# Optimization experiments

Measured on AMD Instinct MI355X. Metric: run time of the kernel, lower is better.

## Reference

```python
import jax, jax.numpy as jnp
import numpy as np

B, S, H = 2, 4096, 1024
WINDOW = 32


def setup_inputs() -> dict:
    key = jax.random.key(0)
    ks = jax.random.split(key, 10)
    s = 1.0 / np.sqrt(H)
    return {
        "hidden_states": jax.random.normal(ks[0], (B, S, H), dtype=jnp.float32),
        "Wq": jax.random.normal(ks[1], (H, H), dtype=jnp.float32) * s,
        "Wk": jax.random.normal(ks[2], (H, H), dtype=jnp.float32) * s,
        "Wv": jax.random.normal(ks[3], (H, H), dtype=jnp.float32) * s,
        "Wo": jax.random.normal(ks[4], (H, H), dtype=jnp.float32) * s,
        "ln_w": jnp.ones((H,), dtype=jnp.float32),
        "ln_b": jnp.zeros((H,), dtype=jnp.float32),
        "W1": jax.random.normal(ks[5], (H // 2, H), dtype=jnp.float32) * s,
        "b1": jnp.zeros((H // 2,), dtype=jnp.float32),
        "W2": jax.random.normal(ks[6], (H, H // 2), dtype=jnp.float32) * (1.0 / np.sqrt(H // 2)),
        "b2": jnp.zeros((H,), dtype=jnp.float32),
    }


def _layernorm(x, w, b, eps=1e-5):
    mu = jnp.mean(x, axis=-1, keepdims=True)
    var = jnp.var(x, axis=-1, keepdims=True)
    return (x - mu) * jax.lax.rsqrt(var + eps) * w + b


def reference(hidden_states, Wq, Wk, Wv, Wo, ln_w, ln_b, W1, b1, W2, b2):
    x = hidden_states  # [B,S,H]
    q = x @ Wq.T
    k = x @ Wk.T
    v = x @ Wv.T
    # banded causal mask: keep j<=i and j >= i-WINDOW+1
    i = jnp.arange(S)[:, None]
    j = jnp.arange(S)[None, :]
    local_mask = (j <= i) & (j >= i - WINDOW + 1)  # [S,S] bool
    scores = jnp.einsum('bqh,bkh->bqk', q, k) / np.sqrt(H)
    scores = jnp.where(local_mask[None], scores, -jnp.inf)
    probs = jax.nn.softmax(scores, axis=-1)
    attn_out = jnp.einsum('bqk,bkh->bqh', probs, v) @ Wo.T
    draft = x + attn_out
    h = _layernorm(draft, ln_w, ln_b)
    h = jax.nn.gelu(h @ W1.T + b1, approximate=False)
    adapter_out = h @ W2.T + b2
    return draft + adapter_out
```

## Files before the change

kernel.cpp:

```cpp
#include <hip/hip_runtime.h>
#include <stdint.h>

typedef unsigned short u16;
typedef __bf16 bfx8 __attribute__((ext_vector_type(8)));
typedef float f32x4 __attribute__((ext_vector_type(4)));

__device__ __forceinline__ u16 f2bf(float x) {
    unsigned int u = __float_as_uint(x);
    u += 0x7fffu + ((u >> 16) & 1u);
    return (u16)(u >> 16);
}

__device__ __forceinline__ void async16(const void* g, void* l) {
    __builtin_amdgcn_global_load_lds(
        (const __attribute__((address_space(1))) unsigned int*)(uintptr_t)g,
        (__attribute__((address_space(3))) unsigned int*)(unsigned int)(uintptr_t)l,
        16, 0, 0);
}

__global__ __launch_bounds__(256) void cast_bf16(const float* __restrict__ in,
                                                 u16* __restrict__ out, int n8) {
    int i = blockIdx.x * 256 + threadIdx.x;
    if (i >= n8) return;
    const float4* p = (const float4*)(in + (size_t)i * 8);
    float4 a = p[0], b = p[1];
    ushort4 o0, o1;
    o0.x = f2bf(a.x); o0.y = f2bf(a.y); o0.z = f2bf(a.z); o0.w = f2bf(a.w);
    o1.x = f2bf(b.x); o1.y = f2bf(b.y); o1.z = f2bf(b.z); o1.w = f2bf(b.w);
    ushort4* q = (ushort4*)(out + (size_t)i * 8);
    q[0] = o0; q[1] = o1;
}

template <int EPI>
__global__ __launch_bounds__(256, 2)
void gemm_nt(const u16* __restrict__ A, const u16* __restrict__ Bw,
             u16* __restrict__ outb, float* __restrict__ outf,
             const float* __restrict__ res, const float* __restrict__ bias,
             int M, int N, int K) {
    __shared__ __align__(1024) unsigned char lds[32768];
    unsigned char* ldsA = lds;
    unsigned char* ldsB = lds + 16384;
    const int t = threadIdx.x;
    const int lane = t & 63, w = t >> 6;
    const int laneR = lane & 15, laneK = lane >> 4;
    const int wr = w >> 1, wc = w & 1;
    const int row0 = blockIdx.y * 128, col0 = blockIdx.x * 128;

    f32x4 acc[4][4] = {};

    int sr[4], sko[4];
#pragma unroll
    for (int c = 0; c < 4; ++c) {
        int li = c * 256 + t;
        sr[c] = li >> 3;
        sko[c] = (li & 7) ^ (sr[c] & 7);
    }

    for (int kt = 0; kt < K; kt += 64) {
#pragma unroll
        for (int c = 0; c < 4; ++c) {
            int li = c * 256 + t;
            async16(A + (size_t)(row0 + sr[c]) * K + kt + sko[c] * 8, ldsA + li * 16);
            async16(Bw + (size_t)(col0 + sr[c]) * K + kt + sko[c] * 8, ldsB + li * 16);
        }
        __syncthreads();
#pragma unroll
        for (int ks = 0; ks < 2; ++ks) {
            bfx8 af[4], bfv[4];
#pragma unroll
            for (int m = 0; m < 4; ++m) {
                int r = wr * 64 + m * 16 + laneR;
                int phys = (ks * 4 + laneK) ^ (r & 7);
                af[m] = *(const bfx8*)(ldsA + r * 128 + phys * 16);
            }
#pragma unroll
            for (int n = 0; n < 4; ++n) {
                int r = wc * 64 + n * 16 + laneR;
                int phys = (ks * 4 + laneK) ^ (r & 7);
                bfv[n] = *(const bfx8*)(ldsB + r * 128 + phys * 16);
            }
#pragma unroll
            for (int m = 0; m < 4; ++m)
#pragma unroll
                for (int n = 0; n < 4; ++n)
                    acc[m][n] = __builtin_amdgcn_mfma_f32_16x16x32_bf16(
                        af[m], bfv[n], acc[m][n], 0, 0, 0);
        }
        __syncthreads();
    }

#pragma unroll
    for (int m = 0; m < 4; ++m) {
#pragma unroll
        for (int n = 0; n < 4; ++n) {
            int gc = col0 + wc * 64 + n * 16 + laneR;
#pragma unroll
            for (int r = 0; r < 4; ++r) {
                int gr = row0 + wr * 64 + m * 16 + laneK * 4 + r;
                size_t idx = (size_t)gr * N + gc;
                float v = acc[m][n][r];
                if constexpr (EPI == 0) {
                    outb[idx] = f2bf(v);
                } else if constexpr (EPI == 1) {
                    outf[idx] = res[idx] + v;
                } else if constexpr (EPI == 2) {
                    float xx = v + bias[gc];
                    outb[idx] = f2bf(xx * 0.5f * (1.0f + erff(xx * 0.70710678118654752f)));
                } else {
                    outf[idx] = res[idx] + v + bias[gc];
                }
            }
        }
    }
}

__global__ __launch_bounds__(256, 2)
void attn_kernel(const u16* __restrict__ Q, const u16* __restrict__ K,
                 const u16* __restrict__ V, u16* __restrict__ O) {
    constexpr int H = 1024, S = 4096;
    const int t = threadIdx.x, lane = t & 63, w = t >> 6;
    const int laneR = lane & 15, laneK = lane >> 4;
    const int tile = blockIdx.x;
    const int batch = tile >> 7;
    const int i0 = (tile & 127) * 32;
    const size_t base = (size_t)batch * S * H;

    __shared__ __align__(16) float S4[4][32][64];
    __shared__ __align__(16) u16 P[32][72];

    f32x4 sc[2][4] = {};
    for (int h = w * 256; h < w * 256 + 256; h += 32) {
        bfx8 qa[2];
#pragma unroll
        for (int m = 0; m < 2; ++m) {
            size_t row = (size_t)(i0 + m * 16 + laneR);
            qa[m] = *(const bfx8*)(Q + base + row * H + h + laneK * 8);
        }
        bfx8 kb[4];
#pragma unroll
        for (int n = 0; n < 4; ++n) {
            int j = i0 - 32 + n * 16 + laneR;
            int jc = j < 0 ? 0 : j;
            kb[n] = *(const bfx8*)(K + base + (size_t)jc * H + h + laneK * 8);
        }
#pragma unroll
        for (int m = 0; m < 2; ++m)
#pragma unroll
            for (int n = 0; n < 4; ++n)
                sc[m][n] = __builtin_amdgcn_mfma_f32_16x16x32_bf16(
                    qa[m], kb[n], sc[m][n], 0, 0, 0);
    }
#pragma unroll
    for (int m = 0; m < 2; ++m)
#pragma unroll
        for (int n = 0; n < 4; ++n)
#pragma unroll
            for (int r = 0; r < 4; ++r)
                S4[w][m * 16 + laneK * 4 + r][n * 16 + laneR] = sc[m][n][r];
    __syncthreads();

    {
        int q = t >> 3;
        int c0 = (t & 7) * 8;
        int lo = q + 1;
        if (32 - i0 > lo) lo = 32 - i0;
        int hi = q + 32;
        float vals[8];
        float mx = -1e30f;
#pragma unroll
        for (int c = 0; c < 8; ++c) {
            int cc = c0 + c;
            float v = (S4[0][q][cc] + S4[1][q][cc] + S4[2][q][cc] + S4[3][q][cc]) * 0.03125f;
            bool valid = (cc >= lo) && (cc <= hi);
            vals[c] = valid ? v : -1e30f;
            if (vals[c] > mx) mx = vals[c];
        }
#pragma unroll
        for (int d = 1; d < 8; d <<= 1) {
            float o = __shfl_xor(mx, d);
            if (o > mx) mx = o;
        }
        float sum = 0.f;
        float es[8];
#pragma unroll
        for (int c = 0; c < 8; ++c) {
            es[c] = (vals[c] > -1e29f) ? __expf(vals[c] - mx) : 0.f;
            sum += es[c];
        }
#pragma unroll
        for (int d = 1; d < 8; d <<= 1) sum += __shfl_xor(sum, d);
        float inv = 1.0f / sum;
#pragma unroll
        for (int c = 0; c < 8; ++c) P[q][c0 + c] = f2bf(es[c] * inv);
    }
    __syncthreads();

    for (int nc = 0; nc < 4; ++nc) {
        int ncol = w * 256 + nc * 64;
        f32x4 o[2][4] = {};
#pragma unroll
        for (int ks = 0; ks < 2; ++ks) {
            bfx8 pa[2];
#pragma unroll
            for (int m = 0; m < 2; ++m)
                pa[m] = *(const bfx8*)(&P[m * 16 + laneR][ks * 32 + laneK * 8]);
#pragma unroll
            for (int n = 0; n < 4; ++n) {
                bfx8 vb;
                int col = ncol + n * 16 + laneR;
                int kb0 = ks * 32 + laneK * 8;
#pragma unroll
                for (int j = 0; j < 8; ++j) {
                    int krow = i0 - 32 + kb0 + j;
                    int kc = krow < 0 ? 0 : krow;
                    vb[j] = *(const __bf16*)(V + base + (size_t)kc * H + col);
                }
#pragma unroll
                for (int m = 0; m < 2; ++m)
                    o[m][n] = __builtin_amdgcn_mfma_f32_16x16x32_bf16(
                        pa[m], vb, o[m][n], 0, 0, 0);
            }
        }
#pragma unroll
        for (int m = 0; m < 2; ++m)
#pragma unroll
            for (int n = 0; n < 4; ++n)
#pragma unroll
                for (int r = 0; r < 4; ++r) {
                    size_t row = (size_t)(i0 + m * 16 + laneK * 4 + r);
                    O[base + row * H + ncol + n * 16 + laneR] = f2bf(o[m][n][r]);
                }
    }
}

__global__ __launch_bounds__(256)
void ln_kernel(const float* __restrict__ x, const float* __restrict__ gw,
               const float* __restrict__ gb, u16* __restrict__ out) {
    const int row = blockIdx.x, t = threadIdx.x;
    const float4 v = ((const float4*)(x + (size_t)row * 1024))[t];
    float s = v.x + v.y + v.z + v.w;
    float s2 = v.x * v.x + v.y * v.y + v.z * v.z + v.w * v.w;
#pragma unroll
    for (int d = 1; d < 64; d <<= 1) {
        s += __shfl_xor(s, d);
        s2 += __shfl_xor(s2, d);
    }
    __shared__ float red[8];
    int lane = t & 63, wv = t >> 6;
    if (lane == 0) { red[wv] = s; red[4 + wv] = s2; }
    __syncthreads();
    float S1 = red[0] + red[1] + red[2] + red[3];
    float S2 = red[4] + red[5] + red[6] + red[7];
    float mu = S1 * (1.0f / 1024.0f);
    float var = S2 * (1.0f / 1024.0f) - mu * mu;
    float rstd = rsqrtf(var + 1e-5f);
    const float4 wv4 = ((const float4*)gw)[t];
    const float4 bv4 = ((const float4*)gb)[t];
    ushort4 o;
    o.x = f2bf((v.x - mu) * rstd * wv4.x + bv4.x);
    o.y = f2bf((v.y - mu) * rstd * wv4.y + bv4.y);
    o.z = f2bf((v.z - mu) * rstd * wv4.z + bv4.z);
    o.w = f2bf((v.w - mu) * rstd * wv4.w + bv4.w);
    ((ushort4*)(out + (size_t)row * 1024))[t] = o;
}

extern "C" void kernel_launch(void* const* d_in, const int* in_sizes, int n_in,
                              void* d_out, int out_size, void* d_ws, size_t ws_size,
                              hipStream_t stream) {
    const float* x   = (const float*)d_in[0];
    const float* Wq  = (const float*)d_in[1];
    const float* Wk  = (const float*)d_in[2];
    const float* Wv  = (const float*)d_in[3];
    const float* Wo  = (const float*)d_in[4];
    const float* lnw = (const float*)d_in[5];
    const float* lnb = (const float*)d_in[6];
    const float* W1  = (const float*)d_in[7];
    const float* b1  = (const float*)d_in[8];
    const float* W2  = (const float*)d_in[9];
    const float* b2  = (const float*)d_in[10];
    (void)in_sizes; (void)n_in; (void)out_size; (void)ws_size; (void)lnb;

    const int M = 8192, H = 1024, Hh = 512;

    char* ws = (char*)d_ws;
    size_t off = 0;
    auto alloc = [&](size_t bytes) {
        char* p = ws + off;
        off += (bytes + 255) & ~(size_t)255;
        return p;
    };
    u16* Xb   = (u16*)alloc((size_t)M * H * 2);
    u16* Wqb  = (u16*)alloc((size_t)H * H * 2);
    u16* Wkb  = (u16*)alloc((size_t)H * H * 2);
    u16* Wvb  = (u16*)alloc((size_t)H * H * 2);
    u16* Wob  = (u16*)alloc((size_t)H * H * 2);
    u16* W1b  = (u16*)alloc((size_t)Hh * H * 2);
    u16* W2b  = (u16*)alloc((size_t)H * Hh * 2);
    u16* Qb   = (u16*)alloc((size_t)M * H * 2);
    u16* Kb   = (u16*)alloc((size_t)M * H * 2);
    u16* Vb   = (u16*)alloc((size_t)M * H * 2);
    float* draft = (float*)alloc((size_t)M * H * 4);
    u16* Attb = Xb;
    u16* hlnb = Qb;
    u16* Gb   = Kb;
    float* outp = (float*)d_out;

    dim3 blk(256);
    auto cast = [&](const float* src, u16* dst, int n) {
        int n8 = n / 8;
        cast_bf16<<<dim3((n8 + 255) / 256), blk, 0, stream>>>(src, dst, n8);
    };
    cast(x, Xb, M * H);
    cast(Wq, Wqb, H * H);
    cast(Wk, Wkb, H * H);
    cast(Wv, Wvb, H * H);
    cast(Wo, Wob, H * H);
    cast(W1, W1b, Hh * H);
    cast(W2, W2b, H * Hh);

    gemm_nt<0><<<dim3(H / 128, M / 128), blk, 0, stream>>>(Xb, Wqb, Qb, nullptr, nullptr, nullptr, M, H, H);
    gemm_nt<0><<<dim3(H / 128, M / 128), blk, 0, stream>>>(Xb, Wkb, Kb, nullptr, nullptr, nullptr, M, H, H);
    gemm_nt<0><<<dim3(H / 128, M / 128), blk, 0, stream>>>(Xb, Wvb, Vb, nullptr, nullptr, nullptr, M, H, H);

    attn_kernel<<<dim3(256), blk, 0, stream>>>(Qb, Kb, Vb, Attb);

    gemm_nt<1><<<dim3(H / 128, M / 128), blk, 0, stream>>>(Attb, Wob, nullptr, draft, x, nullptr, M, H, H);

    ln_kernel<<<dim3(M), blk, 0, stream>>>(draft, lnw, lnb, hlnb);

    gemm_nt<2><<<dim3(Hh / 128, M / 128), blk, 0, stream>>>(hlnb, W1b, Gb, nullptr, nullptr, b1, M, Hh, H);
    gemm_nt<3><<<dim3(H / 128, M / 128), blk, 0, stream>>>(Gb, W2b, nullptr, outp, draft, b2, M, H, Hh);
}
```

Before: 205.0 us.

## Pipeline GEMM with triple-buffered LDS, fuse QKV projection, transpose V for attention

The GEMM becomes a 512-thread, 256x128-tile kernel. It triple-buffers LDS and issues async global-to-LDS prefetch two k-tiles ahead, gated by explicit vmcnt waits and s_barrier, with MFMA priority raised via setprio. The three Q/K/V projections are fused into one GEMM over a concatenated weight. Its epilogue writes V transposed, so attention can load contiguous 8-element vectors instead of 8 strided scalar loads. The seven cast launches are merged into one segmented kernel. The 144KB LDS footprint limits each CU to one block, trading occupancy for deeper software pipelining.

```diff
diff --git a/kernel.cpp b/kernel.cpp
--- a/kernel.cpp
+++ b/kernel.cpp
@@ -18,96 +18,155 @@
         16, 0, 0);
 }
 
-__global__ __launch_bounds__(256) void cast_bf16(const float* __restrict__ in,
-                                                 u16* __restrict__ out, int n8) {
-    int i = blockIdx.x * 256 + threadIdx.x;
-    if (i >= n8) return;
-    const float4* p = (const float4*)(in + (size_t)i * 8);
-    float4 a = p[0], b = p[1];
+#define S_BARRIER() asm volatile("s_barrier" ::: "memory")
+#define WAIT_VM(n) asm volatile("s_waitcnt vmcnt(" #n ")" ::: "memory")
+
+struct CastArgs {
+    const float* src[7];
+    u16* dst[7];
+    int nblk[7];
+};
+__global__ __launch_bounds__(256) void cast_all(CastArgs a) {
+    int b = blockIdx.x, seg = 0;
+    while (b >= a.nblk[seg]) { b -= a.nblk[seg]; ++seg; }
+    int i = b * 256 + threadIdx.x;
+    const float4* p = (const float4*)(a.src[seg] + (size_t)i * 8);
+    float4 x = p[0], y = p[1];
     ushort4 o0, o1;
-    o0.x = f2bf(a.x); o0.y = f2bf(a.y); o0.z = f2bf(a.z); o0.w = f2bf(a.w);
-    o1.x = f2bf(b.x); o1.y = f2bf(b.y); o1.z = f2bf(b.z); o1.w = f2bf(b.w);
-    ushort4* q = (ushort4*)(out + (size_t)i * 8);
+    o0.x = f2bf(x.x); o0.y = f2bf(x.y); o0.z = f2bf(x.z); o0.w = f2bf(x.w);
+    o1.x = f2bf(y.x); o1.y = f2bf(y.y); o1.z = f2bf(y.z); o1.w = f2bf(y.w);
+    ushort4* q = (ushort4*)(a.dst[seg] + (size_t)i * 8);
     q[0] = o0; q[1] = o1;
 }
 
 template <int EPI>
-__global__ __launch_bounds__(256, 2)
+__global__ __launch_bounds__(512, 2)
 void gemm_nt(const u16* __restrict__ A, const u16* __restrict__ Bw,
              u16* __restrict__ outb, float* __restrict__ outf,
              const float* __restrict__ res, const float* __restrict__ bias,
-             int M, int N, int K) {
-    __shared__ __align__(1024) unsigned char lds[32768];
-    unsigned char* ldsA = lds;
-    unsigned char* ldsB = lds + 16384;
+             u16* __restrict__ outq, u16* __restrict__ outk,
+             u16* __restrict__ vt, int M, int N, int K) {
+    __shared__ __align__(1024) unsigned char lds[147456];
     const int t = threadIdx.x;
     const int lane = t & 63, w = t >> 6;
     const int laneR = lane & 15, laneK = lane >> 4;
     const int wr = w >> 1, wc = w & 1;
-    const int row0 = blockIdx.y * 128, col0 = blockIdx.x * 128;
+    const int row0 = blockIdx.y * 256, col0 = blockIdx.x * 128;
+    const int nt = K >> 6;
 
     f32x4 acc[4][4] = {};
 
-    int sr[4], sko[4];
-#pragma unroll
-    for (int c = 0; c < 4; ++c) {
-        int li = c * 256 + t;
-        sr[c] = li >> 3;
-        sko[c] = (li & 7) ^ (sr[c] & 7);
-    }
-
-    for (int kt = 0; kt < K; kt += 64) {
-#pragma unroll
-        for (int c = 0; c < 4; ++c) {
-            int li = c * 256 + t;
-            async16(A + (size_t)(row0 + sr[c]) * K + kt + sko[c] * 8, ldsA + li * 16);
-            async16(Bw + (size_t)(col0 + sr[c]) * K + kt + sko[c] * 8, ldsB + li * 16);
-        }
-        __syncthreads();
+    const u16* srcA[4];
+    const u16* srcB[2];
+    unsigned dA[4], dB[2];
+#pragma unroll
+    for (int i = 0; i < 4; ++i) {
+        int li = i * 512 + t;
+        int row = li >> 3, ko = li & 7;
+        srcA[i] = A + (size_t)(row0 + row) * K + (ko ^ (row & 7)) * 8;
+        dA[i] = li * 16;
+    }
+#pragma unroll
+    for (int i = 0; i < 2; ++i) {
+        int li = i * 512 + t;
+        int row = li >> 3, ko = li & 7;
+        srcB[i] = Bw + (size_t)(col0 + row) * K + (ko ^ (row & 7)) * 8;
+        dB[i] = 32768 + li * 16;
+    }
+
+    auto stage = [&](int b, int tk, int h) {
+        unsigned char* base = lds + b * 49152;
+        const int o = tk * 64;
+        if (h == 0) {
+            async16(srcA[0] + o, base + dA[0]);
+            async16(srcA[1] + o, base + dA[1]);
+            async16(srcB[0] + o, base + dB[0]);
+        } else {
+            async16(srcA[2] + o, base + dA[2]);
+            async16(srcA[3] + o, base + dA[3]);
+            async16(srcB[1] + o, base + dB[1]);
+        }
+    };
+
+    stage(0, 0, 0); stage(0, 0, 1);
+    stage(1, 1, 0); stage(1, 1, 1);
+
+    for (int tk = 0; tk < nt; ++tk) {
+        unsigned char* bufA = lds + (tk % 3) * 49152;
+        unsigned char* bufB = bufA + 32768;
+        if (tk + 1 < nt) { WAIT_VM(6); } else { WAIT_VM(0); }
+        S_BARRIER();
+        const bool pf = (tk + 2 < nt);
+        const int nb = (tk + 2) % 3;
 #pragma unroll
         for (int ks = 0; ks < 2; ++ks) {
-            bfx8 af[4], bfv[4];
+            bfx8 af[4], bf[4];
 #pragma unroll
             for (int m = 0; m < 4; ++m) {
                 int r = wr * 64 + m * 16 + laneR;
                 int phys = (ks * 4 + laneK) ^ (r & 7);
-                af[m] = *(const bfx8*)(ldsA + r * 128 + phys * 16);
+                af[m] = *(const bfx8*)(bufA + r * 128 + phys * 16);
             }
 #pragma unroll
             for (int n = 0; n < 4; ++n) {
                 int r = wc * 64 + n * 16 + laneR;
                 int phys = (ks * 4 + laneK) ^ (r & 7);
-                bfv[n] = *(const bfx8*)(ldsB + r * 128 + phys * 16);
+                bf[n] = *(const bfx8*)(bufB + r * 128 + phys * 16);
             }
+            if (pf) stage(nb, tk + 2, ks);
+            S_BARRIER();
+            __builtin_amdgcn_s_setprio(1);
 #pragma unroll
             for (int m = 0; m < 4; ++m)
 #pragma unroll
                 for (int n = 0; n < 4; ++n)
                     acc[m][n] = __builtin_amdgcn_mfma_f32_16x16x32_bf16(
-                        af[m], bfv[n], acc[m][n], 0, 0, 0);
-        }
-        __syncthreads();
+                        af[m], bf[n], acc[m][n], 0, 0, 0);
+            __builtin_amdgcn_s_setprio(0);
+            S_BARRIER();
+        }
     }
 
 #pragma unroll
     for (int m = 0; m < 4; ++m) {
+        const int gr0 = row0 + wr * 64 + m * 16 + laneK * 4;
 #pragma unroll
         for (int n = 0; n < 4; ++n) {
-            int gc = col0 + wc * 64 + n * 16 + laneR;
-#pragma unroll
-            for (int r = 0; r < 4; ++r) {
-                int gr = row0 + wr * 64 + m * 16 + laneK * 4 + r;
-                size_t idx = (size_t)gr * N + gc;
-                float v = acc[m][n][r];
-                if constexpr (EPI == 0) {
-                    outb[idx] = f2bf(v);
-                } else if constexpr (EPI == 1) {
-                    outf[idx] = res[idx] + v;
-                } else if constexpr (EPI == 2) {
-                    float xx = v + bias[gc];
-                    outb[idx] = f2bf(xx * 0.5f * (1.0f + erff(xx * 0.70710678118654752f)));
+            const int gc = col0 + wc * 64 + n * 16 + laneR;
+            if constexpr (EPI == 0) {
+                if (col0 < 1024) {
+#pragma unroll
+                    for (int r = 0; r < 4; ++r)
+                        outq[(size_t)(gr0 + r) * 1024 + gc] = f2bf(acc[m][n][r]);
+                } else if (col0 < 2048) {
+#pragma unroll
+                    for (int r = 0; r < 4; ++r)
+                        outk[(size_t)(gr0 + r) * 1024 + (gc - 1024)] = f2bf(acc[m][n][r]);
                 } else {
-                    outf[idx] = res[idx] + v + bias[gc];
+                    ushort4 o4;
+                    o4.x = f2bf(acc[m][n][0]); o4.y = f2bf(acc[m][n][1]);
+                    o4.z = f2bf(acc[m][n][2]); o4.w = f2bf(acc[m][n][3]);
+                    *(ushort4*)(vt + (((size_t)(gr0 >> 12)) * 1024 + (gc - 2048)) * 4096 +
+                                (gr0 & 4095)) = o4;
+                }
+            } else if constexpr (EPI == 1) {
+#pragma unroll
+                for (int r = 0; r < 4; ++r) {
+                    size_t idx = (size_t)(gr0 + r) * N + gc;
+                    outf[idx] = res[idx] + acc[m][n][r];
+                }
+            } else if constexpr (EPI == 2) {
+#pragma unroll
+                for (int r = 0; r < 4; ++r) {
+                    float xx = acc[m][n][r] + bias[gc];
+                    outb[(size_t)(gr0 + r) * N + gc] =
+                        f2bf(xx * 0.5f * (1.0f + erff(xx * 0.70710678118654752f)));
+                }
+            } else {
+#pragma unroll
+                for (int r = 0; r < 4; ++r) {
+                    size_t idx = (size_t)(gr0 + r) * N + gc;
+                    outf[idx] = res[idx] + acc[m][n][r] + bias[gc];
                 }
             }
         }
@@ -116,7 +175,7 @@
 
 __global__ __launch_bounds__(256, 2)
 void attn_kernel(const u16* __restrict__ Q, const u16* __restrict__ K,
-                 const u16* __restrict__ V, u16* __restrict__ O) {
+                 const u16* __restrict__ vt, u16* __restrict__ O) {
     constexpr int H = 1024, S = 4096;
     const int t = threadIdx.x, lane = t & 63, w = t >> 6;
     const int laneR = lane & 15, laneK = lane >> 4;
@@ -204,17 +263,12 @@
 #pragma unroll
             for (int m = 0; m < 2; ++m)
                 pa[m] = *(const bfx8*)(&P[m * 16 + laneR][ks * 32 + laneK * 8]);
+            int t0 = i0 - 32 + ks * 32 + laneK * 8;
+            if (t0 < 0) t0 = 0;
 #pragma unroll
             for (int n = 0; n < 4; ++n) {
-                bfx8 vb;
-                int col = ncol + n * 16 + laneR;
-                int kb0 = ks * 32 + laneK * 8;
-#pragma unroll
-                for (int j = 0; j < 8; ++j) {
-                    int krow = i0 - 32 + kb0 + j;
-                    int kc = krow < 0 ? 0 : krow;
-                    vb[j] = *(const __bf16*)(V + base + (size_t)kc * H + col);
-                }
+                int c = ncol + n * 16 + laneR;
+                bfx8 vb = *(const bfx8*)(vt + ((size_t)batch * 1024 + c) * 4096 + t0);
 #pragma unroll
                 for (int m = 0; m < 2; ++m)
                     o[m][n] = __builtin_amdgcn_mfma_f32_16x16x32_bf16(
@@ -278,7 +332,7 @@
     const float* b1  = (const float*)d_in[8];
     const float* W2  = (const float*)d_in[9];
     const float* b2  = (const float*)d_in[10];
-    (void)in_sizes; (void)n_in; (void)out_size; (void)ws_size; (void)lnb;
+    (void)in_sizes; (void)n_in; (void)out_size; (void)ws_size;
 
     const int M = 8192, H = 1024, Hh = 512;
 
@@ -289,45 +343,46 @@
         off += (bytes + 255) & ~(size_t)255;
         return p;
     };
-    u16* Xb   = (u16*)alloc((size_t)M * H * 2);
-    u16* Wqb  = (u16*)alloc((size_t)H * H * 2);
-    u16* Wkb  = (u16*)alloc((size_t)H * H * 2);
-    u16* Wvb  = (u16*)alloc((size_t)H * H * 2);
-    u16* Wob  = (u16*)alloc((size_t)H * H * 2);
-    u16* W1b  = (u16*)alloc((size_t)Hh * H * 2);
-    u16* W2b  = (u16*)alloc((size_t)H * Hh * 2);
-    u16* Qb   = (u16*)alloc((size_t)M * H * 2);
-    u16* Kb   = (u16*)alloc((size_t)M * H * 2);
-    u16* Vb   = (u16*)alloc((size_t)M * H * 2);
+    u16* Xb    = (u16*)alloc((size_t)M * H * 2);
+    u16* Wqkvb = (u16*)alloc((size_t)3 * H * H * 2);
+    u16* Wob   = (u16*)alloc((size_t)H * H * 2);
+    u16* W1b   = (u16*)alloc((size_t)Hh * H * 2);
+    u16* W2b   = (u16*)alloc((size_t)H * Hh * 2);
+    u16* Qb    = (u16*)alloc((size_t)M * H * 2);
+    u16* Kb    = (u16*)alloc((size_t)M * H * 2);
+    u16* Vt    = (u16*)alloc((size_t)M * H * 2);
     float* draft = (float*)alloc((size_t)M * H * 4);
     u16* Attb = Xb;
     u16* hlnb = Qb;
     u16* Gb   = Kb;
     float* outp = (float*)d_out;
 
-    dim3 blk(256);
-    auto cast = [&](const float* src, u16* dst, int n) {
-        int n8 = n / 8;
-        cast_bf16<<<dim3((n8 + 255) / 256), blk, 0, stream>>>(src, dst, n8);
-    };
-    cast(x, Xb, M * H);
-    cast(Wq, Wqb, H * H);
-    cast(Wk, Wkb, H * H);
-    cast(Wv, Wvb, H * H);
-    cast(Wo, Wob, H * H);
-    cast(W1, W1b, Hh * H);
-    cast(W2, W2b, H * Hh);
-
-    gemm_nt<0><<<dim3(H / 128, M / 128), blk, 0, stream>>>(Xb, Wqb, Qb, nullptr, nullptr, nullptr, M, H, H);
-    gemm_nt<0><<<dim3(H / 128, M / 128), blk, 0, stream>>>(Xb, Wkb, Kb, nullptr, nullptr, nullptr, M, H, H);
-    gemm_nt<0><<<dim3(H / 128, M / 128), blk, 0, stream>>>(Xb, Wvb, Vb, nullptr, nullptr, nullptr, M, H, H);
-
-    attn_kernel<<<dim3(256), blk, 0, stream>>>(Qb, Kb, Vb, Attb);
-
-    gemm_nt<1><<<dim3(H / 128, M / 128), blk, 0, stream>>>(Attb, Wob, nullptr, draft, x, nullptr, M, H, H);
-
-    ln_kernel<<<dim3(M), blk, 0, stream>>>(draft, lnw, lnb, hlnb);
-
-    gemm_nt<2><<<dim3(Hh / 128, M / 128), blk, 0, stream>>>(hlnb, W1b, Gb, nullptr, nullptr, b1, M, Hh, H);
-    gemm_nt<3><<<dim3(H / 128, M / 128), blk, 0, stream>>>(Gb, W2b, nullptr, outp, draft, b2, M, H, Hh);
-}
+    CastArgs ca;
+    ca.src[0] = x;  ca.dst[0] = Xb;                   ca.nblk[0] = (M * H / 8) / 256;
+    ca.src[1] = Wq; ca.dst[1] = Wqkvb;                ca.nblk[1] = (H * H / 8) / 256;
+    ca.src[2] = Wk; ca.dst[2] = Wqkvb + (size_t)H * H;     ca.nblk[2] = (H * H / 8) / 256;
+    ca.src[3] = Wv; ca.dst[3] = Wqkvb + (size_t)2 * H * H; ca.nblk[3] = (H * H / 8) / 256;
+    ca.src[4] = Wo; ca.dst[4] = Wob;                  ca.nblk[4] = (H * H / 8) / 256;
+    ca.src[5] = W1; ca.dst[5] = W1b;                  ca.nblk[5] = (Hh * H / 8) / 256;
+    ca.src[6] = W2; ca.dst[6] = W2b;                  ca.nblk[6] = (H * Hh / 8) / 256;
+    int totblk = 0;
+    for (int i = 0; i < 7; ++i) totblk += ca.nblk[i];
+    cast_all<<<dim3(totblk), dim3(256), 0, stream>>>(ca);
+
+    dim3 gblk(512);
+    gemm_nt<0><<<dim3(3 * H / 128, M / 256), gblk, 0, stream>>>(
+        Xb, Wqkvb, nullptr, nullptr, nullptr, nullptr, Qb, Kb, Vt, M, 3 * H, H);
+
+    attn_kernel<<<dim3(256), dim3(256), 0, stream>>>(Qb, Kb, Vt, Attb);
+
+    gemm_nt<1><<<dim3(H / 128, M / 256), gblk, 0, stream>>>(
+        Attb, Wob, nullptr, draft, x, nullptr, nullptr, nullptr, nullptr, M, H, H);
+
+    ln_kernel<<<dim3(M), dim3(256), 0, stream>>>(draft, lnw, lnb, hlnb);
+
+    gemm_nt<2><<<dim3(Hh / 128, M / 256), gblk, 0, stream>>>(
+        hlnb, W1b, Gb, nullptr, nullptr, b1, nullptr, nullptr, nullptr, M, Hh, H);
+
+    gemm_nt<3><<<dim3(H / 128, M / 256), gblk, 0, stream>>>(
+        Gb, W2b, nullptr, outp, draft, b2, nullptr, nullptr, nullptr, M, H, Hh);
+}
```

Measured after the change: 190.6 us. 7.0% less time.
